# Optimization experiments

Measured on AMD Instinct MI355X. Metric: run time of the kernel, lower is better.

Reference implementation:

```python
import jax, jax.numpy as jnp
import numpy as np

NUM_TOKENS = 256; MAX_SEQ = 512; DIM = 512; NL = 8; NH = 8; FF = 2048; NC = 4; P = 16
E = DIM // NH  # head dim = 64


def layernorm(x, g, b, eps=1e-5):
    m = jnp.mean(x, -1, keepdims=True)
    v = jnp.var(x, -1, keepdims=True)
    return (x - m) / jnp.sqrt(v + eps) * g + b


def rotary_cos_sin(S):
    inv = 1.0 / (10000.0 ** (jnp.arange(0, E, 2, dtype=jnp.float32) / E))
    f = jnp.arange(S, dtype=jnp.float32)[:, None] * inv[None, :]  # [S, E/2]
    emb = jnp.concatenate([f, f], -1)                             # [S, E]
    return jnp.cos(emb)[None, :, None, :], jnp.sin(emb)[None, :, None, :]


def rotate_half(x):
    x1, x2 = jnp.split(x, 2, axis=-1)
    return jnp.concatenate([-x2, x1], -1)


def apply_rot(x, cos, sin):
    return x * cos + rotate_half(x) * sin


def linear_attention(q, k, v, key_mask, eps=1e-6):
    # fast_transformers LinearAttention: phi(x) = elu(x) + 1, non-causal
    Q = jax.nn.elu(q) + 1.0
    K = (jax.nn.elu(k) + 1.0) * key_mask[:, :, None, None]
    KV = jnp.einsum('nshd,nshm->nhmd', K, v)
    Z = 1.0 / (jnp.einsum('nlhd,nhd->nlh', Q, K.sum(1)) + eps)
    return jnp.einsum('nlhd,nhmd,nlh->nlhm', Q, KV, Z)


def setup_inputs() -> dict:
    key = jax.random.key(0)
    ks = jax.random.split(key, 24)
    N, Ltok = 32, 4096
    nrm = lambda k, s: jax.random.normal(k, s, dtype=jnp.float32) * 0.02
    inp = {}
    inp['inputs'] = jax.random.normal(ks[0], (N, Ltok, NUM_TOKENS), dtype=jnp.float32)
    inp['input_mask'] = jnp.ones((N, Ltok), dtype=jnp.float32)
    inp['cond'] = jax.random.randint(ks[1], (N,), 0, NC)
    inp['emb_W'] = nrm(ks[2], (NUM_TOKENS, DIM)); inp['emb_b'] = jnp.zeros((DIM,), jnp.float32)
    inp['conv_W'] = nrm(ks[3], (DIM, DIM, P)); inp['conv_b'] = jnp.zeros((DIM,), jnp.float32)
    inp['pos_emb'] = nrm(ks[4], (MAX_SEQ, DIM))
    inp['cls_token'] = jax.random.normal(ks[5], (1, 1, DIM), dtype=jnp.float32)
    inp['Wq'] = nrm(ks[6], (NL, DIM, DIM)); inp['bq'] = jnp.zeros((NL, DIM), jnp.float32)
    inp['Wk'] = nrm(ks[7], (NL, DIM, DIM)); inp['bk'] = jnp.zeros((NL, DIM), jnp.float32)
    inp['Wv'] = nrm(ks[8], (NL, DIM, DIM)); inp['bv'] = jnp.zeros((NL, DIM), jnp.float32)
    inp['Wo'] = nrm(ks[9], (NL, DIM, DIM)); inp['bo'] = jnp.zeros((NL, DIM), jnp.float32)
    inp['ln1_g'] = jnp.ones((NL, DIM), jnp.float32); inp['ln1_b'] = jnp.zeros((NL, DIM), jnp.float32)
    inp['W1'] = nrm(ks[10], (NL, DIM, FF)); inp['b1'] = jnp.zeros((NL, FF), jnp.float32)
    inp['W2'] = nrm(ks[11], (NL, FF, DIM)); inp['b2'] = jnp.zeros((NL, DIM), jnp.float32)
    inp['ln2_g'] = jnp.ones((NL, DIM), jnp.float32); inp['ln2_b'] = jnp.zeros((NL, DIM), jnp.float32)
    inp['normf_g'] = jnp.ones((DIM,), jnp.float32); inp['normf_b'] = jnp.zeros((DIM,), jnp.float32)
    inp['cond_emb'] = nrm(ks[12], (NC + 1, DIM))
    inp['outg_W'] = nrm(ks[13], (DIM, 1)); inp['outg_b'] = jnp.zeros((1,), jnp.float32)
    inp['outl_W'] = nrm(ks[14], (DIM, 1)); inp['outl_b'] = jnp.zeros((1,), jnp.float32)
    return inp


def reference(emb_W, emb_b, conv_W, conv_b, pos_emb, cls_token,
              Wq, bq, Wk, bk, Wv, bv, Wo, bo, ln1_g, ln1_b,
              W1, b1, W2, b2, ln2_g, ln2_b, normf_g, normf_b,
              cond_emb, outg_W, outg_b, outl_W, outl_b,
              inputs, input_mask, cond):
    N, Ltok, _ = inputs.shape
    x = inputs @ emb_W + emb_b                                   # [N, L, D]
    # Conv1d(D, D, P, stride=P) == per-patch projection
    xr = x.reshape(N, Ltok // P, P, DIM)
    x = jnp.einsum('ntpd,odp->nto', xr, conv_W) + conv_b         # [N, Pn, D]
    cls = jnp.broadcast_to(cls_token, (N, 1, DIM))
    x = jnp.concatenate([cls, x], 1)                             # [N, S, D]
    S = x.shape[1]
    mask_full = jnp.concatenate([jnp.ones((N, 1), input_mask.dtype), input_mask], 1)
    x = x + pos_emb[:S][None]
    mask_len = jnp.ceil(jnp.sum(mask_full, -1) / P)
    key_mask = (jnp.arange(S)[None, :] < mask_len[:, None]).astype(x.dtype)
    cos, sin = rotary_cos_sin(S)
    for i in range(NL):
        q = (x @ Wq[i] + bq[i]).reshape(N, S, NH, E)
        k = (x @ Wk[i] + bk[i]).reshape(N, S, NH, E)
        v = (x @ Wv[i] + bv[i]).reshape(N, S, NH, E)
        q = apply_rot(q, cos, sin)
        k = apply_rot(k, cos, sin)
        a = linear_attention(q, k, v, key_mask).reshape(N, S, DIM)
        a = a @ Wo[i] + bo[i]
        y = layernorm(x + a, ln1_g[i], ln1_b[i])                 # post-norm (fast_transformers)
        f = jax.nn.gelu(y @ W1[i] + b1[i], approximate=False) @ W2[i] + b2[i]
        x = layernorm(y + f, ln2_g[i], ln2_b[i])
    x = layernorm(x, normf_g, normf_b)
    out_class = x[:, 0]                                          # [N, D]
    out_global = out_class @ outg_W + outg_b                     # [N, 1]
    out_seq = x[:, 1:]                                           # [N, S-1, D]
    out_local = out_seq @ outl_W + outl_b                        # [N, S-1, 1]
    ce = cond_emb[cond]                                          # [N, D]
    out_global = out_global + jnp.sum(ce * out_class, -1, keepdims=True)
    out_local = out_local + jnp.sum(ce[:, None, :] * out_seq, -1, keepdims=True)
    return out_global, out_local
```

## Files before the change

### kernel.cpp

```cpp
#include <hip/hip_runtime.h>

typedef __attribute__((ext_vector_type(4))) float f32x4;
typedef __attribute__((ext_vector_type(8))) __bf16 bf16x8;

#define SEQ   257
#define NBATCH 32
#define DIMD  512
#define FFD   2048
#define NLYR  8
#define MROWS (NBATCH*SEQ)
#define MPAD  8320
#define MSTEM 8192
#define KSTEM 4096
#define QKVD  1536

__device__ __forceinline__ unsigned short f2bf(float f) {
  unsigned int u = __float_as_uint(f);
  return (unsigned short)((u + 0x7FFFu + ((u >> 16) & 1u)) >> 16);
}
__device__ __forceinline__ float bf2f(unsigned short u) {
  return __uint_as_float(((unsigned int)u) << 16);
}
__device__ __forceinline__ float elu1(float x) { return x > 0.f ? x + 1.f : expf(x); }

__device__ __forceinline__ void gload16(const void* g, void* l) {
  __builtin_amdgcn_global_load_lds((__attribute__((address_space(1))) void*)g,
                                   (__attribute__((address_space(3))) void*)l, 16, 0, 0);
}

template<int EPI>
__global__ __launch_bounds__(256)
void gemm_bt(const unsigned short* __restrict__ A,
             const unsigned short* __restrict__ BT,
             const float* __restrict__ bias,
             void* __restrict__ Cout, int K, int Nn, int NBY) {
  constexpr int MW = 2;
  constexpr int NW = 4;
  constexpr int BM = 128;
  constexpr int BN = 64;
  __shared__ __align__(16) unsigned short sA[2][BM * 64];
  __shared__ __align__(16) unsigned short sB[2][BN * 64];
  const int tid = threadIdx.x;
  const int w = tid >> 6, l = tid & 63;
  const int nwg = gridDim.x;
  const int q = nwg >> 3, r = nwg & 7;
  const int xcd = blockIdx.x & 7, idx = blockIdx.x >> 3;
  const int wg = (xcd < r) ? (xcd * (q + 1) + idx) : (r * (q + 1) + (xcd - r) * q + idx);
  const int bx = wg / NBY, by = wg % NBY;
  const long tm = (long)bx * BM;
  const long tn = (long)by * BN;
  const int lr = l & 15, lg = l >> 4;
  const int lr7 = lr & 7;

  auto stage = [&](int buf, int t) {
    const long k0 = (long)t * 64;
#pragma unroll
    for (int j = 0; j < BM * 8 / 256; ++j) {
      const int ch = j * 256 + tid;
      const int rr = ch >> 3, s = ch & 7;
      gload16(A + (tm + rr) * (long)K + k0 + ((s ^ (rr & 7)) * 8), sA[buf] + ch * 8);
    }
#pragma unroll
    for (int j = 0; j < BN * 8 / 256; ++j) {
      const int ch = j * 256 + tid;
      const int rr = ch >> 3, s = ch & 7;
      gload16(BT + (tn + rr) * (long)K + k0 + ((s ^ (rr & 7)) * 8), sB[buf] + ch * 8);
    }
  };

  f32x4 acc[MW][NW];
#pragma unroll
  for (int m = 0; m < MW; ++m)
#pragma unroll
    for (int n = 0; n < NW; ++n) acc[m][n] = (f32x4){0.f, 0.f, 0.f, 0.f};

  const int nt = K >> 6;
  stage(0, 0);
  for (int t = 0; t < nt; ++t) {
    const int cur = t & 1;
    __syncthreads();
    if (t + 1 < nt) stage(cur ^ 1, t + 1);
#pragma unroll
    for (int kk = 0; kk < 2; ++kk) {
      const int sl = ((lg + kk * 4) ^ lr7) * 8;
      bf16x8 af[MW], bfr[NW];
#pragma unroll
      for (int m = 0; m < MW; ++m)
        af[m] = *(const bf16x8*)(sA[cur] + (w * MW * 16 + m * 16 + lr) * 64 + sl);
#pragma unroll
      for (int n = 0; n < NW; ++n)
        bfr[n] = *(const bf16x8*)(sB[cur] + (n * 16 + lr) * 64 + sl);
#pragma unroll
      for (int m = 0; m < MW; ++m)
#pragma unroll
        for (int n = 0; n < NW; ++n)
          acc[m][n] = __builtin_amdgcn_mfma_f32_16x16x32_bf16(af[m], bfr[n], acc[m][n], 0, 0, 0);
    }
  }
#pragma unroll
  for (int m = 0; m < MW; ++m) {
    const long gr0 = tm + w * MW * 16 + m * 16 + lg * 4;
#pragma unroll
    for (int n = 0; n < NW; ++n) {
      const long gc = tn + n * 16 + lr;
      const float bv = bias ? bias[gc] : 0.f;
#pragma unroll
      for (int j = 0; j < 4; ++j) {
        float v = acc[m][n][j] + bv;
        if (EPI == 0) {
          ((float*)Cout)[(gr0 + j) * (long)Nn + gc] = v;
        } else if (EPI == 1) {
          float g = 0.5f * v * (1.f + erff(v * 0.70710678118f));
          ((unsigned short*)Cout)[(gr0 + j) * (long)Nn + gc] = f2bf(g);
        } else {
          ((unsigned short*)Cout)[(gr0 + j) * (long)Nn + gc] = f2bf(v);
        }
      }
    }
  }
}

template<int OUT_BF>
__global__ void transpose_k(const float* __restrict__ src, void* __restrict__ dst,
                            int K, int N, long dstZ) {
  __shared__ float t[32][33];
  const long lz = blockIdx.z;
  const float* S = src + lz * (long)K * N;
  const long k0 = (long)blockIdx.x * 32, n0 = (long)blockIdx.y * 32;
  for (int i = threadIdx.y; i < 32; i += 8)
    t[i][threadIdx.x] = S[(k0 + i) * (long)N + n0 + threadIdx.x];
  __syncthreads();
  for (int i = threadIdx.y; i < 32; i += 8) {
    long o = lz * dstZ + (n0 + i) * (long)K + k0 + threadIdx.x;
    float val = t[threadIdx.x][i];
    if (OUT_BF) ((unsigned short*)dst)[o] = f2bf(val);
    else ((float*)dst)[o] = val;
  }
}

__global__ __launch_bounds__(256)
void weff_kernel(const float* __restrict__ embWT, const float* __restrict__ convW,
                 const float* __restrict__ emb_b, const float* __restrict__ conv_b,
                 unsigned short* __restrict__ WeT, float* __restrict__ bias2) {
  __shared__ float sc[8192];
  const int o = blockIdx.x;
  const float* C = convW + (long)o * 8192;
  for (int i = threadIdx.x; i < 8192; i += 256) sc[i] = C[i];
  __syncthreads();
  const int c = threadIdx.x;
  float acc[16];
#pragma unroll
  for (int p = 0; p < 16; ++p) acc[p] = 0.f;
  for (int d = 0; d < 512; ++d) {
    float ev = embWT[d * 256 + c];
#pragma unroll
    for (int p = 0; p < 16; ++p) acc[p] += ev * sc[d * 16 + p];
  }
#pragma unroll
  for (int p = 0; p < 16; ++p) WeT[(long)o * 4096 + p * 256 + c] = f2bf(acc[p]);
  float lb = 0.f;
  for (int d = c; d < 512; d += 256) {
    float s16 = 0.f;
#pragma unroll
    for (int p = 0; p < 16; ++p) s16 += sc[d * 16 + p];
    lb += emb_b[d] * s16;
  }
#pragma unroll
  for (int of = 1; of < 64; of <<= 1) lb += __shfl_xor(lb, of, 64);
  __shared__ float red[4];
  if ((threadIdx.x & 63) == 0) red[threadIdx.x >> 6] = lb;
  __syncthreads();
  if (threadIdx.x == 0) bias2[o] = red[0] + red[1] + red[2] + red[3] + conv_b[o];
}

__global__ void f32_to_bf16_k(const float* __restrict__ in, unsigned short* __restrict__ out, long n4) {
  long i = (long)blockIdx.x * blockDim.x + threadIdx.x;
  const long stride = (long)gridDim.x * blockDim.x;
  for (; i < n4; i += stride) {
    float4 v = ((const float4*)in)[i];
    ushort4 o; o.x = f2bf(v.x); o.y = f2bf(v.y); o.z = f2bf(v.z); o.w = f2bf(v.w);
    ((ushort4*)out)[i] = o;
  }
}

__global__ void rotary_k(float* __restrict__ cosT, float* __restrict__ sinT) {
  int idx = blockIdx.x * 256 + threadIdx.x;
  if (idx >= SEQ * 32) return;
  int s = idx >> 5, j = idx & 31;
  float inv = expf(-(float)(2 * j) * (1.f / 64.f) * 9.210340371976184f);
  float a = (float)s * inv;
  cosT[idx] = cosf(a);
  sinT[idx] = sinf(a);
}

__global__ void concat_bias_k(const float* __restrict__ bq, const float* __restrict__ bk,
                              const float* __restrict__ bv, float* __restrict__ bqkv) {
  int idx = blockIdx.x * 256 + threadIdx.x;
  if (idx >= NLYR * QKVD) return;
  int i = idx / QKVD, j = idx % QKVD;
  float v;
  if (j < 512) v = bq[i * 512 + j];
  else if (j < 1024) v = bk[i * 512 + j - 512];
  else v = bv[i * 512 + j - 1024];
  bqkv[idx] = v;
}

__global__ __launch_bounds__(256)
void masklen_k(const float* __restrict__ mask, float* __restrict__ mlen) {
  int n = blockIdx.x;
  float s = 0.f;
  for (int i = threadIdx.x; i < 4096; i += 256) s += mask[(long)n * 4096 + i];
#pragma unroll
  for (int of = 1; of < 64; of <<= 1) s += __shfl_xor(s, of, 64);
  __shared__ float red[4];
  if ((threadIdx.x & 63) == 0) red[threadIdx.x >> 6] = s;
  __syncthreads();
  if (threadIdx.x == 0) mlen[n] = ceilf((1.f + red[0] + red[1] + red[2] + red[3]) * (1.f / 16.f));
}

__global__ void assemble_x(const float* __restrict__ stem, const float* __restrict__ bias2,
                           const float* __restrict__ posemb, const float* __restrict__ cls,
                           float* __restrict__ Xf, unsigned short* __restrict__ Xbf) {
  long idx = (long)blockIdx.x * 256 + threadIdx.x;
  if (idx >= (long)MROWS * 128) return;
  long row = idx >> 7;
  int c4 = (int)(idx & 127) * 4;
  int n = (int)(row / SEQ), s = (int)(row % SEQ);
  float4 p = *(const float4*)(posemb + (long)s * DIMD + c4);
  float4 v;
  if (s == 0) {
    float4 cv = *(const float4*)(cls + c4);
    v.x = cv.x + p.x; v.y = cv.y + p.y; v.z = cv.z + p.z; v.w = cv.w + p.w;
  } else {
    float4 st = *(const float4*)(stem + ((long)(n * 256 + s - 1)) * DIMD + c4);
    float4 b2 = *(const float4*)(bias2 + c4);
    v.x = st.x + b2.x + p.x; v.y = st.y + b2.y + p.y; v.z = st.z + b2.z + p.z; v.w = st.w + b2.w + p.w;
  }
  *(float4*)(Xf + row * DIMD + c4) = v;
  ushort4 o; o.x = f2bf(v.x); o.y = f2bf(v.y); o.z = f2bf(v.z); o.w = f2bf(v.w);
  *(ushort4*)(Xbf + row * DIMD + c4) = o;
}

__global__ __launch_bounds__(256)
void attn_fused_k(const unsigned short* __restrict__ QKV,
                  const float* __restrict__ cosT, const float* __restrict__ sinT,
                  const float* __restrict__ mlen, unsigned short* __restrict__ Obf) {
  const int n = blockIdx.x >> 3, h = blockIdx.x & 7;
  __shared__ __align__(16) unsigned short sKT[64 * 64];
  __shared__ __align__(16) unsigned short sVT[80 * 64];
  __shared__ __align__(16) unsigned short sKVT[80 * 64];
  __shared__ __align__(16) unsigned short sQ[64 * 64];
  const int t = threadIdx.x;
  const int w = t >> 6, ln = t & 63;
  const int lr = ln & 15, lg = ln >> 4;
  const int lr7 = lr & 7;
  const float mlen_n = mlen[n];

  {
    unsigned short val = (t < 16) ? (unsigned short)0x3F80 : (unsigned short)0;
    ushort4 iv; iv.x = val; iv.y = val; iv.z = val; iv.w = val;
    *(ushort4*)(sVT + 64 * 64 + t * 4) = iv;
  }

  f32x4 accA[5];
#pragma unroll
  for (int mt = 0; mt < 5; ++mt) accA[mt] = (f32x4){0.f, 0.f, 0.f, 0.f};

  for (int ch = 0; ch < 5; ++ch) {
#pragma unroll
    for (int pass = 0; pass < 4; ++pass) {
      const int slot = pass * 256 + t;
      const int sl_ = slot >> 4;
      const int j = slot & 15;
      const int c0 = 2 * j;
      const int srow = ch * 64 + sl_;
      float kr0 = 0.f, kr1 = 0.f, kr2 = 0.f, kr3 = 0.f;
      float v0 = 0.f, v1 = 0.f, v2 = 0.f, v3 = 0.f;
      if (srow < SEQ) {
        const unsigned short* Rw = QKV + ((long)(n * SEQ + srow)) * QKVD + h * 64;
        ushort2 ka = *(const ushort2*)(Rw + 512 + c0);
        ushort2 kb = *(const ushort2*)(Rw + 512 + c0 + 32);
        ushort2 va = *(const ushort2*)(Rw + 1024 + c0);
        ushort2 vb = *(const ushort2*)(Rw + 1024 + c0 + 32);
        float c0v = cosT[srow * 32 + c0], c1v = cosT[srow * 32 + c0 + 1];
        float s0v = sinT[srow * 32 + c0], s1v = sinT[srow * 32 + c0 + 1];
        float km = ((float)srow < mlen_n) ? 1.f : 0.f;
        float ka0 = bf2f(ka.x), ka1 = bf2f(ka.y), kb0 = bf2f(kb.x), kb1 = bf2f(kb.y);
        kr0 = elu1(ka0 * c0v - kb0 * s0v) * km;
        kr1 = elu1(ka1 * c1v - kb1 * s1v) * km;
        kr2 = elu1(kb0 * c0v + ka0 * s0v) * km;
        kr3 = elu1(kb1 * c1v + ka1 * s1v) * km;
        v0 = bf2f(va.x); v1 = bf2f(va.y); v2 = bf2f(vb.x); v3 = bf2f(vb.y);
      }
      const int sh = sl_ >> 3, slow = sl_ & 7;
      sKT[(c0)      * 64 + (((sh ^ ((c0)      & 7)) << 3) | slow)] = f2bf(kr0);
      sKT[(c0 + 1)  * 64 + (((sh ^ ((c0 + 1)  & 7)) << 3) | slow)] = f2bf(kr1);
      sKT[(c0 + 32) * 64 + (((sh ^ ((c0 + 32) & 7)) << 3) | slow)] = f2bf(kr2);
      sKT[(c0 + 33) * 64 + (((sh ^ ((c0 + 33) & 7)) << 3) | slow)] = f2bf(kr3);
      sVT[(c0)      * 64 + (((sh ^ ((c0)      & 7)) << 3) | slow)] = f2bf(v0);
      sVT[(c0 + 1)  * 64 + (((sh ^ ((c0 + 1)  & 7)) << 3) | slow)] = f2bf(v1);
      sVT[(c0 + 32) * 64 + (((sh ^ ((c0 + 32) & 7)) << 3) | slow)] = f2bf(v2);
      sVT[(c0 + 33) * 64 + (((sh ^ ((c0 + 33) & 7)) << 3) | slow)] = f2bf(v3);
    }
    __syncthreads();
#pragma unroll
    for (int kk = 0; kk < 2; ++kk) {
      const int sl = ((lg + kk * 4) ^ lr7) * 8;
      bf16x8 bk = *(const bf16x8*)(sKT + (w * 16 + lr) * 64 + sl);
#pragma unroll
      for (int mt = 0; mt < 5; ++mt) {
        bf16x8 av = *(const bf16x8*)(sVT + (mt * 16 + lr) * 64 + sl);
        accA[mt] = __builtin_amdgcn_mfma_f32_16x16x32_bf16(av, bk, accA[mt], 0, 0, 0);
      }
    }
    __syncthreads();
  }
  {
    const int d = w * 16 + lr;
    const int dh = d >> 3, dlow = d & 7;
#pragma unroll
    for (int mt = 0; mt < 5; ++mt) {
#pragma unroll
      for (int j = 0; j < 4; ++j) {
        const int m = mt * 16 + lg * 4 + j;
        sKVT[m * 64 + (((dh ^ (m & 7)) << 3) | dlow)] = f2bf(accA[mt][j]);
      }
    }
  }
  __syncthreads();

  for (int qt = 0; qt < 5; ++qt) {
#pragma unroll
    for (int pass = 0; pass < 4; ++pass) {
      const int slot = pass * 256 + t;
      const int ll = slot >> 4;
      const int j = slot & 15;
      const int c0 = 2 * j;
      int lq = qt * 64 + ll;
      const int lqc = (lq < SEQ) ? lq : (SEQ - 1);
      const unsigned short* Rw = QKV + ((long)(n * SEQ + lqc)) * QKVD + h * 64;
      ushort2 qa = *(const ushort2*)(Rw + c0);
      ushort2 qb = *(const ushort2*)(Rw + c0 + 32);
      float c0v = cosT[lqc * 32 + c0], c1v = cosT[lqc * 32 + c0 + 1];
      float s0v = sinT[lqc * 32 + c0], s1v = sinT[lqc * 32 + c0 + 1];
      float a0 = bf2f(qa.x), a1 = bf2f(qa.y), b0 = bf2f(qb.x), b1 = bf2f(qb.y);
      float q0 = elu1(a0 * c0v - b0 * s0v);
      float q1 = elu1(a1 * c1v - b1 * s1v);
      float q2 = elu1(b0 * c0v + a0 * s0v);
      float q3 = elu1(b1 * c1v + a1 * s1v);
      const int l7 = ll & 7;
      ushort2 p0; p0.x = f2bf(q0); p0.y = f2bf(q1);
      ushort2 p1; p1.x = f2bf(q2); p1.y = f2bf(q3);
      *(ushort2*)(sQ + ll * 64 + ((((c0 >> 3) ^ l7) << 3) | (c0 & 7))) = p0;
      *(ushort2*)(sQ + ll * 64 + (((((c0 + 32) >> 3) ^ l7) << 3) | (c0 & 7))) = p1;
    }
    __syncthreads();
    f32x4 accB[5];
#pragma unroll
    for (int nt = 0; nt < 5; ++nt) accB[nt] = (f32x4){0.f, 0.f, 0.f, 0.f};
#pragma unroll
    for (int kk = 0; kk < 2; ++kk) {
      const int sl = ((lg + kk * 4) ^ lr7) * 8;
      bf16x8 aq = *(const bf16x8*)(sQ + (w * 16 + lr) * 64 + sl);
#pragma unroll
      for (int nt = 0; nt < 5; ++nt) {
        bf16x8 bkv = *(const bf16x8*)(sKVT + (nt * 16 + lr) * 64 + sl);
        accB[nt] = __builtin_amdgcn_mfma_f32_16x16x32_bf16(aq, bkv, accB[nt], 0, 0, 0);
      }
    }
#pragma unroll
    for (int j = 0; j < 4; ++j) {
      float z = __shfl(accB[4][j], ln & 48, 64);
      float zr = 1.f / (z + 1e-6f);
      const int lq = qt * 64 + w * 16 + lg * 4 + j;
      if (lq < SEQ) {
        const long orow = ((long)(n * SEQ + lq)) * DIMD + h * 64;
#pragma unroll
        for (int nt = 0; nt < 4; ++nt)
          Obf[orow + nt * 16 + lr] = f2bf(accB[nt][j] * zr);
      }
    }
    __syncthreads();
  }
}

__global__ __launch_bounds__(128)
void add_ln_k(const float* __restrict__ X, const unsigned short* __restrict__ A,
              const float* __restrict__ g, const float* __restrict__ b,
              float* __restrict__ Yf, unsigned short* __restrict__ Ybf) {
  int row = blockIdx.x, t = threadIdx.x;
  long base = (long)row * DIMD + t * 4;
  float4 xv = *(const float4*)(X + base);
  ushort4 au = *(const ushort4*)(A + base);
  float4 s;
  s.x = xv.x + bf2f(au.x); s.y = xv.y + bf2f(au.y);
  s.z = xv.z + bf2f(au.z); s.w = xv.w + bf2f(au.w);
  float sum = s.x + s.y + s.z + s.w;
  float sq = s.x * s.x + s.y * s.y + s.z * s.z + s.w * s.w;
#pragma unroll
  for (int of = 1; of < 64; of <<= 1) { sum += __shfl_xor(sum, of, 64); sq += __shfl_xor(sq, of, 64); }
  __shared__ float red[4];
  if ((t & 63) == 0) { red[(t >> 6) * 2] = sum; red[(t >> 6) * 2 + 1] = sq; }
  __syncthreads();
  sum = red[0] + red[2]; sq = red[1] + red[3];
  float mean = sum * (1.f / 512.f);
  float var = sq * (1.f / 512.f) - mean * mean;
  float rstd = rsqrtf(var + 1e-5f);
  float4 gv = *(const float4*)(g + t * 4);
  float4 bv = *(const float4*)(b + t * 4);
  float4 y;
  y.x = (s.x - mean) * rstd * gv.x + bv.x;
  y.y = (s.y - mean) * rstd * gv.y + bv.y;
  y.z = (s.z - mean) * rstd * gv.z + bv.z;
  y.w = (s.w - mean) * rstd * gv.w + bv.w;
  *(float4*)(Yf + base) = y;
  ushort4 o; o.x = f2bf(y.x); o.y = f2bf(y.y); o.z = f2bf(y.z); o.w = f2bf(y.w);
  *(ushort4*)(Ybf + base) = o;
}

__global__ __launch_bounds__(128)
void final_head_k(const float* __restrict__ X, const float* __restrict__ g, const float* __restrict__ b,
                  const float* __restrict__ condemb, const int* __restrict__ cond,
                  const float* __restrict__ outgW, const float* __restrict__ outgb,
                  const float* __restrict__ outlW, const float* __restrict__ outlb,
                  float* __restrict__ out) {
  int row = blockIdx.x, t = threadIdx.x;
  int n = row / SEQ, s = row % SEQ;
  long base = (long)row * DIMD + t * 4;
  float4 xv = *(const float4*)(X + base);
  float sum = xv.x + xv.y + xv.z + xv.w;
  float sq = xv.x * xv.x + xv.y * xv.y + xv.z * xv.z + xv.w * xv.w;
#pragma unroll
  for (int of = 1; of < 64; of <<= 1) { sum += __shfl_xor(sum, of, 64); sq += __shfl_xor(sq, of, 64); }
  __shared__ float red[4];
  if ((t & 63) == 0) { red[(t >> 6) * 2] = sum; red[(t >> 6) * 2 + 1] = sq; }
  __syncthreads();
  sum = red[0] + red[2]; sq = red[1] + red[3];
  float mean = sum * (1.f / 512.f);
  float var = sq * (1.f / 512.f) - mean * mean;
  float rstd = rsqrtf(var + 1e-5f);
  float4 gv = *(const float4*)(g + t * 4);
  float4 bv = *(const float4*)(b + t * 4);
  const float* wsel = (s == 0) ? outgW : outlW;
  const float* ce = condemb + (long)cond[n] * DIMD;
  float4 wv = *(const float4*)(wsel + t * 4);
  float4 cv = *(const float4*)(ce + t * 4);
  float l0 = (xv.x - mean) * rstd * gv.x + bv.x;
  float l1 = (xv.y - mean) * rstd * gv.y + bv.y;
  float l2 = (xv.z - mean) * rstd * gv.z + bv.z;
  float l3 = (xv.w - mean) * rstd * gv.w + bv.w;
  float pl = l0 * wv.x + l1 * wv.y + l2 * wv.z + l3 * wv.w;
  float pc = l0 * cv.x + l1 * cv.y + l2 * cv.z + l3 * cv.w;
#pragma unroll
  for (int of = 1; of < 64; of <<= 1) { pl += __shfl_xor(pl, of, 64); pc += __shfl_xor(pc, of, 64); }
  __shared__ float red2[4];
  if ((t & 63) == 0) { red2[(t >> 6) * 2] = pl; red2[(t >> 6) * 2 + 1] = pc; }
  __syncthreads();
  if (t == 0) {
    float res = red2[0] + red2[2] + red2[1] + red2[3] + ((s == 0) ? outgb[0] : outlb[0]);
    long oi = (s == 0) ? (long)n : (32 + (long)n * 256 + (s - 1));
    out[oi] = res;
  }
}

extern "C" void kernel_launch(void* const* d_in, const int* in_sizes, int n_in,
                              void* d_out, int out_size, void* d_ws, size_t ws_size,
                              hipStream_t stream) {
  const float* inputs    = (const float*)d_in[0];
  const float* input_mask= (const float*)d_in[1];
  const int*   cond      = (const int*)d_in[2];
  const float* emb_W     = (const float*)d_in[3];
  const float* emb_b     = (const float*)d_in[4];
  const float* conv_W    = (const float*)d_in[5];
  const float* conv_b    = (const float*)d_in[6];
  const float* pos_emb   = (const float*)d_in[7];
  const float* cls_token = (const float*)d_in[8];
  const float* Wq = (const float*)d_in[9];   const float* bq = (const float*)d_in[10];
  const float* Wk = (const float*)d_in[11];  const float* bk = (const float*)d_in[12];
  const float* Wv = (const float*)d_in[13];  const float* bv = (const float*)d_in[14];
  const float* Wo = (const float*)d_in[15];  const float* bo = (const float*)d_in[16];
  const float* ln1_g = (const float*)d_in[17]; const float* ln1_b = (const float*)d_in[18];
  const float* W1 = (const float*)d_in[19];  const float* b1 = (const float*)d_in[20];
  const float* W2 = (const float*)d_in[21];  const float* b2 = (const float*)d_in[22];
  const float* ln2_g = (const float*)d_in[23]; const float* ln2_b = (const float*)d_in[24];
  const float* normf_g = (const float*)d_in[25]; const float* normf_b = (const float*)d_in[26];
  const float* cond_emb = (const float*)d_in[27];
  const float* outg_W = (const float*)d_in[28]; const float* outg_b = (const float*)d_in[29];
  const float* outl_W = (const float*)d_in[30]; const float* outl_b = (const float*)d_in[31];

  char* ws = (char*)d_ws;
  size_t off = 0;
  auto alloc = [&](size_t bytes) -> char* {
    char* p = ws + off;
    off += (bytes + 255) & ~(size_t)255;
    return p;
  };
  unsigned short* WeT   = (unsigned short*)alloc((size_t)512 * 4096 * 2);
  float*          embWT = (float*)alloc((size_t)512 * 256 * 4);
  float*          bias2 = (float*)alloc(512 * 4);
  float*          cosT  = (float*)alloc(SEQ * 32 * 4);
  float*          sinT  = (float*)alloc(SEQ * 32 * 4);
  float*          mlen  = (float*)alloc(32 * 4);
  unsigned short* Wqkv  = (unsigned short*)alloc((size_t)NLYR * QKVD * 512 * 2);
  float*          bqkv  = (float*)alloc((size_t)NLYR * QKVD * 4);
  unsigned short* WoT = (unsigned short*)alloc((size_t)NLYR * 512 * 512 * 2);
  unsigned short* W1T = (unsigned short*)alloc((size_t)NLYR * 2048 * 512 * 2);
  unsigned short* W2T = (unsigned short*)alloc((size_t)NLYR * 512 * 2048 * 2);
  char*           big  = alloc((size_t)MSTEM * KSTEM * 2);
  unsigned short* in_bf   = (unsigned short*)big;
  unsigned short* tqkv_bf = (unsigned short*)big;
  float*          x_f  = (float*)alloc((size_t)MPAD * DIMD * 4);
  unsigned short* x_bf = (unsigned short*)alloc((size_t)MPAD * DIMD * 2);
  float*          y_f  = (float*)alloc((size_t)MPAD * DIMD * 4);
  unsigned short* y_bf = (unsigned short*)alloc((size_t)MPAD * DIMD * 2);
  float*          t0   = (float*)alloc((size_t)MPAD * DIMD * 4);
  unsigned short* t0bf = (unsigned short*)alloc((size_t)MPAD * DIMD * 2);
  unsigned short* attn_bf = (unsigned short*)alloc((size_t)MPAD * DIMD * 2);
  unsigned short* h_bf = (unsigned short*)alloc((size_t)MPAD * FFD * 2);
  (void)ws_size; (void)in_sizes; (void)n_in; (void)out_size;

  dim3 tb(32, 8);
  transpose_k<1><<<dim3(16, 16, 8), tb, 0, stream>>>(Wq, Wqkv, 512, 512, (long)QKVD * 512);
  transpose_k<1><<<dim3(16, 16, 8), tb, 0, stream>>>(Wk, Wqkv + (size_t)512 * 512, 512, 512, (long)QKVD * 512);
  transpose_k<1><<<dim3(16, 16, 8), tb, 0, stream>>>(Wv, Wqkv + (size_t)1024 * 512, 512, 512, (long)QKVD * 512);
  transpose_k<1><<<dim3(16, 16, 8), tb, 0, stream>>>(Wo, WoT, 512, 512, (long)512 * 512);
  transpose_k<1><<<dim3(16, 64, 8), tb, 0, stream>>>(W1, W1T, 512, 2048, (long)512 * 2048);
  transpose_k<1><<<dim3(64, 16, 8), tb, 0, stream>>>(W2, W2T, 2048, 512, (long)2048 * 512);
  transpose_k<0><<<dim3(8, 16, 1), tb, 0, stream>>>(emb_W, embWT, 256, 512, 0);
  concat_bias_k<<<(NLYR * QKVD + 255) / 256, 256, 0, stream>>>(bq, bk, bv, bqkv);
  weff_kernel<<<512, 256, 0, stream>>>(embWT, conv_W, emb_b, conv_b, WeT, bias2);
  f32_to_bf16_k<<<4096, 256, 0, stream>>>(inputs, in_bf, (long)MSTEM * KSTEM / 4);
  rotary_k<<<(SEQ * 32 + 255) / 256, 256, 0, stream>>>(cosT, sinT);
  masklen_k<<<32, 256, 0, stream>>>(input_mask, mlen);

  gemm_bt<0><<<512, 256, 0, stream>>>(in_bf, WeT, nullptr, t0, KSTEM, DIMD, 8);
  assemble_x<<<(MROWS * 128 + 255) / 256, 256, 0, stream>>>(t0, bias2, pos_emb, cls_token, x_f, x_bf);

  for (int i = 0; i < NLYR; ++i) {
    const unsigned short* wqkv = Wqkv + (size_t)i * QKVD * 512;
    const unsigned short* wo = WoT + (size_t)i * 512 * 512;
    const unsigned short* w1 = W1T + (size_t)i * 2048 * 512;
    const unsigned short* w2 = W2T + (size_t)i * 512 * 2048;
    gemm_bt<2><<<65 * 24, 256, 0, stream>>>(x_bf, wqkv, bqkv + i * QKVD, tqkv_bf, 512, QKVD, 24);
    attn_fused_k<<<256, 256, 0, stream>>>(tqkv_bf, cosT, sinT, mlen, attn_bf);
    gemm_bt<2><<<65 * 8, 256, 0, stream>>>(attn_bf, wo, bo + i * 512, t0bf, 512, 512, 8);
    add_ln_k<<<MROWS, 128, 0, stream>>>(x_f, t0bf, ln1_g + i * 512, ln1_b + i * 512, y_f, y_bf);
    gemm_bt<1><<<65 * 32, 256, 0, stream>>>(y_bf, w1, b1 + i * 2048, h_bf, 512, 2048, 32);
    gemm_bt<2><<<65 * 8, 256, 0, stream>>>(h_bf, w2, b2 + i * 512, t0bf, 2048, 512, 8);
    add_ln_k<<<MROWS, 128, 0, stream>>>(y_f, t0bf, ln2_g + i * 512, ln2_b + i * 512, x_f, x_bf);
  }
  final_head_k<<<MROWS, 128, 0, stream>>>(x_f, normf_g, normf_b, cond_emb, cond,
                                          outg_W, outg_b, outl_W, outl_b, (float*)d_out);
}
```

Measured before the change: 1.491 ms.

## Add triple-buffered GEMM with explicit vmcnt waits for long-K GEMMs

Adds a gemm_bt_p3 kernel that keeps three shared-memory stages in flight, waiting with explicit s_waitcnt vmcnt counts and raw barriers in place of __syncthreads. It is used for the stem GEMM (K=4096) and the FFN down-projection (K=2048), where the long K loop should benefit most from deeper prefetch. The intent is to hide global load latency better. In exchange, shared memory per block grows by half, which may lower occupancy, and the hand-counted vmcnt values are tied to exactly six loads per stage. The stage loop counts in the original kernel are also hardcoded to 4 and 2.

```diff
diff --git a/kernel.cpp b/kernel.cpp
--- a/kernel.cpp
+++ b/kernel.cpp
@@ -55,13 +55,13 @@
   auto stage = [&](int buf, int t) {
     const long k0 = (long)t * 64;
 #pragma unroll
-    for (int j = 0; j < BM * 8 / 256; ++j) {
+    for (int j = 0; j < 4; ++j) {
       const int ch = j * 256 + tid;
       const int rr = ch >> 3, s = ch & 7;
       gload16(A + (tm + rr) * (long)K + k0 + ((s ^ (rr & 7)) * 8), sA[buf] + ch * 8);
     }
 #pragma unroll
-    for (int j = 0; j < BN * 8 / 256; ++j) {
+    for (int j = 0; j < 2; ++j) {
       const int ch = j * 256 + tid;
       const int rr = ch >> 3, s = ch & 7;
       gload16(BT + (tn + rr) * (long)K + k0 + ((s ^ (rr & 7)) * 8), sB[buf] + ch * 8);
@@ -97,6 +97,117 @@
           acc[m][n] = __builtin_amdgcn_mfma_f32_16x16x32_bf16(af[m], bfr[n], acc[m][n], 0, 0, 0);
     }
   }
+#pragma unroll
+  for (int m = 0; m < MW; ++m) {
+    const long gr0 = tm + w * MW * 16 + m * 16 + lg * 4;
+#pragma unroll
+    for (int n = 0; n < NW; ++n) {
+      const long gc = tn + n * 16 + lr;
+      const float bv = bias ? bias[gc] : 0.f;
+#pragma unroll
+      for (int j = 0; j < 4; ++j) {
+        float v = acc[m][n][j] + bv;
+        if (EPI == 0) {
+          ((float*)Cout)[(gr0 + j) * (long)Nn + gc] = v;
+        } else if (EPI == 1) {
+          float g = 0.5f * v * (1.f + erff(v * 0.70710678118f));
+          ((unsigned short*)Cout)[(gr0 + j) * (long)Nn + gc] = f2bf(g);
+        } else {
+          ((unsigned short*)Cout)[(gr0 + j) * (long)Nn + gc] = f2bf(v);
+        }
+      }
+    }
+  }
+}
+
+template<int EPI>
+__global__ __launch_bounds__(256)
+void gemm_bt_p3(const unsigned short* __restrict__ A,
+                const unsigned short* __restrict__ BT,
+                const float* __restrict__ bias,
+                void* __restrict__ Cout, int K, int Nn, int NBY) {
+  constexpr int MW = 2;
+  constexpr int NW = 4;
+  constexpr int BM = 128;
+  constexpr int BN = 64;
+  __shared__ __align__(16) unsigned short sA[3][BM * 64];
+  __shared__ __align__(16) unsigned short sB[3][BN * 64];
+  const int tid = threadIdx.x;
+  const int w = tid >> 6, l = tid & 63;
+  const int nwg = gridDim.x;
+  const int q = nwg >> 3, r = nwg & 7;
+  const int xcd = blockIdx.x & 7, idx = blockIdx.x >> 3;
+  const int wg = (xcd < r) ? (xcd * (q + 1) + idx) : (r * (q + 1) + (xcd - r) * q + idx);
+  const int bx = wg / NBY, by = wg % NBY;
+  const long tm = (long)bx * BM;
+  const long tn = (long)by * BN;
+  const int lr = l & 15, lg = l >> 4;
+  const int lr7 = lr & 7;
+
+  auto stage = [&](int buf, int t) {
+    const long k0 = (long)t * 64;
+#pragma unroll
+    for (int j = 0; j < 4; ++j) {
+      const int ch = j * 256 + tid;
+      const int rr = ch >> 3, s = ch & 7;
+      gload16(A + (tm + rr) * (long)K + k0 + ((s ^ (rr & 7)) * 8), sA[buf] + ch * 8);
+    }
+#pragma unroll
+    for (int j = 0; j < 2; ++j) {
+      const int ch = j * 256 + tid;
+      const int rr = ch >> 3, s = ch & 7;
+      gload16(BT + (tn + rr) * (long)K + k0 + ((s ^ (rr & 7)) * 8), sB[buf] + ch * 8);
+    }
+  };
+
+  f32x4 acc[MW][NW];
+#pragma unroll
+  for (int m = 0; m < MW; ++m)
+#pragma unroll
+    for (int n = 0; n < NW; ++n) acc[m][n] = (f32x4){0.f, 0.f, 0.f, 0.f};
+
+  auto compute = [&](int buf) {
+#pragma unroll
+    for (int kk = 0; kk < 2; ++kk) {
+      const int sl = ((lg + kk * 4) ^ lr7) * 8;
+      bf16x8 af[MW], bfr[NW];
+#pragma unroll
+      for (int m = 0; m < MW; ++m)
+        af[m] = *(const bf16x8*)(sA[buf] + (w * MW * 16 + m * 16 + lr) * 64 + sl);
+#pragma unroll
+      for (int n = 0; n < NW; ++n)
+        bfr[n] = *(const bf16x8*)(sB[buf] + (n * 16 + lr) * 64 + sl);
+#pragma unroll
+      for (int m = 0; m < MW; ++m)
+#pragma unroll
+        for (int n = 0; n < NW; ++n)
+          acc[m][n] = __builtin_amdgcn_mfma_f32_16x16x32_bf16(af[m], bfr[n], acc[m][n], 0, 0, 0);
+    }
+  };
+
+  const int nt = K >> 6;
+  stage(0, 0);
+  stage(1, 1);
+  stage(2, 2);
+  int t = 0;
+  for (; t < nt - 2; ++t) {
+    asm volatile("s_waitcnt vmcnt(12)" ::: "memory");
+    __builtin_amdgcn_s_barrier();
+    __builtin_amdgcn_sched_barrier(0);
+    compute(t % 3);
+    __builtin_amdgcn_s_barrier();
+    if (t + 3 < nt) stage(t % 3, t + 3);
+  }
+  asm volatile("s_waitcnt vmcnt(6)" ::: "memory");
+  __builtin_amdgcn_s_barrier();
+  __builtin_amdgcn_sched_barrier(0);
+  compute((nt - 2) % 3);
+  __builtin_amdgcn_s_barrier();
+  asm volatile("s_waitcnt vmcnt(0)" ::: "memory");
+  __builtin_amdgcn_s_barrier();
+  __builtin_amdgcn_sched_barrier(0);
+  compute((nt - 1) % 3);
+
 #pragma unroll
   for (int m = 0; m < MW; ++m) {
     const long gr0 = tm + w * MW * 16 + m * 16 + lg * 4;
@@ -533,7 +644,7 @@
   rotary_k<<<(SEQ * 32 + 255) / 256, 256, 0, stream>>>(cosT, sinT);
   masklen_k<<<32, 256, 0, stream>>>(input_mask, mlen);
 
-  gemm_bt<0><<<512, 256, 0, stream>>>(in_bf, WeT, nullptr, t0, KSTEM, DIMD, 8);
+  gemm_bt_p3<0><<<512, 256, 0, stream>>>(in_bf, WeT, nullptr, t0, KSTEM, DIMD, 8);
   assemble_x<<<(MROWS * 128 + 255) / 256, 256, 0, stream>>>(t0, bias2, pos_emb, cls_token, x_f, x_bf);
 
   for (int i = 0; i < NLYR; ++i) {
@@ -546,7 +657,7 @@
     gemm_bt<2><<<65 * 8, 256, 0, stream>>>(attn_bf, wo, bo + i * 512, t0bf, 512, 512, 8);
     add_ln_k<<<MROWS, 128, 0, stream>>>(x_f, t0bf, ln1_g + i * 512, ln1_b + i * 512, y_f, y_bf);
     gemm_bt<1><<<65 * 32, 256, 0, stream>>>(y_bf, w1, b1 + i * 2048, h_bf, 512, 2048, 32);
-    gemm_bt<2><<<65 * 8, 256, 0, stream>>>(h_bf, w2, b2 + i * 512, t0bf, 2048, 512, 8);
+    gemm_bt_p3<2><<<65 * 8, 256, 0, stream>>>(h_bf, w2, b2 + i * 512, t0bf, 2048, 512, 8);
     add_ln_k<<<MROWS, 128, 0, stream>>>(y_f, t0bf, ln2_g + i * 512, ln2_b + i * 512, x_f, x_bf);
   }
   final_head_k<<<MROWS, 128, 0, stream>>>(x_f, normf_g, normf_b, cond_emb, cond,
```

Result: slower. 1.637 ms (+9.8%).
